# Kernel tuning notes

Hardware: AMD Instinct MI355X
Metric: run time of the kernel (lower is better)

Reference implementation:

```python
import jax, jax.numpy as jnp
import numpy as np

S, N, M, D = 4, 4096, 4096, 128
NEG = -1e30
EPS = 1e-12


def setup_inputs() -> dict:
    key = jax.random.key(0)
    k1, k2, k3 = jax.random.split(key, 3)
    art = jax.random.normal(k1, (S, N, D), dtype=jnp.float32)
    ref = jax.random.normal(k2, (S, M, D), dtype=jnp.float32)
    pos_mask = jax.random.randint(k3, (S, N, M), 0, 2).astype(jnp.bool_)
    log_temperature = jnp.log(jnp.asarray(0.01, dtype=jnp.float32))
    return {"art": art, "ref": ref, "pos_mask": pos_mask, "log_temperature": log_temperature}


def _l2norm(x):
    # F.normalize: x / max(||x||, eps)
    n = jnp.sqrt(jnp.sum(x * x, axis=-1, keepdims=True))
    return x / jnp.maximum(n, EPS)


def reference(art, ref, pos_mask, log_temperature):
    temp = jnp.exp(log_temperature)
    a = _l2norm(art)                                   # [S,N,D]
    r = _l2norm(ref)                                   # [S,M,D]
    logits = jnp.einsum("snd,smd->snm", a, r) / temp   # [S,N,M]

    den = jax.nn.logsumexp(logits, axis=-1)                              # [S,N]
    num = jax.nn.logsumexp(jnp.where(pos_mask, logits, NEG), axis=-1)    # [S,N]

    n_pos = jnp.sum(pos_mask, axis=-1)                 # [S,N]
    n_ref = logits.shape[-1]
    valid = (n_pos > 0) & (n_ref > n_pos)              # skip anchors with 0 pos or all pos

    per_anchor = den - num                             # -(num - den)
    cnt = jnp.sum(valid, axis=-1)                      # [S]
    stem_loss = jnp.sum(jnp.where(valid, per_anchor, 0.0), axis=-1) / jnp.maximum(cnt, 1)
    stem_valid = cnt > 0
    loss = jnp.sum(jnp.where(stem_valid, stem_loss, 0.0)) / jnp.maximum(jnp.sum(stem_valid), 1)
    return loss
```

## Files before the change

kernel.cpp:

```cpp
#include <hip/hip_runtime.h>
#include <hip/hip_bf16.h>
#include <math.h>

#define S_ 4
#define N_ 4096
#define M_ 4096
#define D_ 128
#define NEG_ (-1e30f)
#define CH_ 2
#define MCH_ (M_ / CH_)
#define NST_ (MCH_ / 64)
#define LN2_ 0.69314718055994531f
#define LOG2E_ 1.44269504088896340f

typedef __bf16 bf16x8 __attribute__((ext_vector_type(8)));
typedef float f32x4 __attribute__((ext_vector_type(4)));

__device__ __forceinline__ void gll16(const void* g, void* l) {
    __builtin_amdgcn_global_load_lds(
        (const __attribute__((address_space(1))) unsigned int*)g,
        (__attribute__((address_space(3))) unsigned int*)l, 16, 0, 0);
}

__device__ __forceinline__ unsigned short f2bf(float f) {
    unsigned u = __float_as_uint(f);
    unsigned r = (u + 0x7FFFu + ((u >> 16) & 1u)) >> 16;
    return (unsigned short)r;
}

__global__ void nrm_rows_kernel(const float* __restrict__ art, const float* __restrict__ ref,
                                unsigned short* __restrict__ an, unsigned short* __restrict__ rn) {
    const int w = threadIdx.x >> 6;
    const int lane = threadIdx.x & 63;
    const int row = blockIdx.x * 4 + w;
    const bool is_art = row < S_ * N_;
    const float* src = is_art ? (art + (size_t)row * D_)
                              : (ref + (size_t)(row - S_ * N_) * D_);
    unsigned short* dst = is_art ? (an + (size_t)row * D_)
                                 : (rn + (size_t)(row - S_ * N_) * D_);
    const float2 v = *reinterpret_cast<const float2*>(src + lane * 2);
    float ss = v.x * v.x + v.y * v.y;
#pragma unroll
    for (int off = 1; off < 64; off <<= 1) ss += __shfl_xor(ss, off);
    const float scale = 1.0f / fmaxf(sqrtf(ss), 1e-12f);
    unsigned pack = (unsigned)f2bf(v.x * scale) | ((unsigned)f2bf(v.y * scale) << 16);
    *reinterpret_cast<unsigned*>(dst + lane * 2) = pack;
}

__global__ __launch_bounds__(256, 4) void infonce_main_kernel(
    const unsigned short* __restrict__ an, const unsigned short* __restrict__ rn,
    const unsigned char* __restrict__ maskb, const float* __restrict__ logtemp,
    float4* __restrict__ part4) {

    const int bid = blockIdx.x;
    const int swz = (bid & 7) * 128 + (bid >> 3);
    const int ch = swz >> 9;
    const int s = (swz >> 7) & 3;
    const int nblk = swz & 127;
    const int n_base = nblk * 32;

    const int tid = threadIdx.x;
    const int w = tid >> 6;
    const int lane = tid & 63;
    const int nsub = w & 1;
    const int msub = w >> 1;
    const int n16 = n_base + nsub * 16;
    const int lrow = lane & 15;
    const int lgrp = lane >> 4;
    const float scale2 = __expf(-logtemp[0]) * LOG2E_;

    const unsigned* mu = (const unsigned*)maskb;
    unsigned pr = 0;
#pragma unroll
    for (int i = 0; i < 4; ++i) pr |= (mu[i * 64 + lane] > 1u) ? 1u : 0u;
    const bool byte_mode = (__ballot(pr != 0) != 0ull);
    const size_t mstride = byte_mode ? 1 : 4;

    __shared__ unsigned char smem[2][64 * 256];
    __shared__ unsigned long long mbuf[2][32];
    __shared__ float4 lds4[4][16];

    bf16x8 bfr[4];
    const unsigned short* abase = an + ((size_t)(s * N_ + n16 + lrow)) * D_ + lgrp * 8;
#pragma unroll
    for (int kc = 0; kc < 4; ++kc)
        bfr[kc] = *reinterpret_cast<const bf16x8*>(abase + kc * 32);

    const int srow = w * 4 + (lane >> 4);
    const int schunk = (lane & 15) ^ (srow & 7);
    const int lane_src_off = srow * 256 + schunk * 16;
    const unsigned char* rn_chunk =
        (const unsigned char*)(rn + ((size_t)(s * M_ + ch * MCH_)) * D_);

    size_t rowb[8];
#pragma unroll
    for (int r = 0; r < 8; ++r)
        rowb[r] = ((size_t)(s * N_ + n_base + w * 8 + r) * M_ + (size_t)ch * MCH_) * mstride;

    const int rb0 = (msub * 32 + lrow) * 256;
    int coff[4];
#pragma unroll
    for (int kc = 0; kc < 4; ++kc) coff[kc] = ((kc * 4 + lgrp) ^ (lrow & 7)) * 16;

    float dmax = NEG_, dsum = 0.f, nsum = 0.f;
    int npos = 0;

    {
        const unsigned char* src = rn_chunk + lane_src_off;
        unsigned char* dst = &smem[0][w * 1024];
#pragma unroll
        for (int j = 0; j < 4; ++j) gll16(src + j * 4096, dst + j * 4096);
        unsigned char mv[8];
        const size_t eoff = (size_t)lane * mstride;
#pragma unroll
        for (int r = 0; r < 8; ++r) mv[r] = maskb[rowb[r] + eoff];
        unsigned long long bl[8];
#pragma unroll
        for (int r = 0; r < 8; ++r) bl[r] = __ballot(mv[r] != 0);
        if (lane == 0) {
#pragma unroll
            for (int r = 0; r < 8; ++r) mbuf[0][w * 8 + r] = bl[r];
        }
    }
    __syncthreads();

    for (int st = 0; st < NST_; ++st) {
        const int nb = st & 1;
        const bool pf = (st + 1 < NST_);
        unsigned char mv[8];
        if (pf) {
            const unsigned char* src = rn_chunk + (size_t)(st + 1) * 16384 + lane_src_off;
            unsigned char* dst = &smem[nb ^ 1][w * 1024];
#pragma unroll
            for (int j = 0; j < 4; ++j) gll16(src + j * 4096, dst + j * 4096);
            const size_t eoff = (size_t)((st + 1) * 64 + lane) * mstride;
#pragma unroll
            for (int r = 0; r < 8; ++r) mv[r] = maskb[rowb[r] + eoff];
        }
        const unsigned char* base = &smem[nb][0] + rb0;
        f32x4 acc0 = {0.f, 0.f, 0.f, 0.f}, acc1 = {0.f, 0.f, 0.f, 0.f};
#pragma unroll
        for (int kc = 0; kc < 4; ++kc) {
            acc0 = __builtin_amdgcn_mfma_f32_16x16x32_bf16(
                *reinterpret_cast<const bf16x8*>(base + coff[kc]), bfr[kc], acc0, 0, 0, 0);
            acc1 = __builtin_amdgcn_mfma_f32_16x16x32_bf16(
                *reinterpret_cast<const bf16x8*>(base + 4096 + coff[kc]), bfr[kc], acc1, 0, 0, 0);
        }
        const unsigned long long wmask = mbuf[nb][nsub * 16 + lrow];
        const unsigned nib0 = (unsigned)(wmask >> (msub * 32 + lgrp * 4)) & 0xFu;
        const unsigned nib1 = (unsigned)(wmask >> (msub * 32 + 16 + lgrp * 4)) & 0xFu;
        float l0 = acc0[0] * scale2, l1 = acc0[1] * scale2, l2 = acc0[2] * scale2, l3 = acc0[3] * scale2;
        float l4 = acc1[0] * scale2, l5 = acc1[1] * scale2, l6 = acc1[2] * scale2, l7 = acc1[3] * scale2;
        float tmax = fmaxf(fmaxf(fmaxf(l0, l1), fmaxf(l2, l3)),
                           fmaxf(fmaxf(l4, l5), fmaxf(l6, l7)));
        const float nmx = fmaxf(dmax, tmax);
        const float r = exp2f(dmax - nmx);
        float e0 = exp2f(l0 - nmx), e1 = exp2f(l1 - nmx), e2 = exp2f(l2 - nmx), e3 = exp2f(l3 - nmx);
        float e4 = exp2f(l4 - nmx), e5 = exp2f(l5 - nmx), e6 = exp2f(l6 - nmx), e7 = exp2f(l7 - nmx);
        dsum = dsum * r + (((e0 + e1) + (e2 + e3)) + ((e4 + e5) + (e6 + e7)));
        float p0 = ((nib0 & 1u) ? e0 : 0.f) + (((nib0 >> 1) & 1u) ? e1 : 0.f);
        float p1 = (((nib0 >> 2) & 1u) ? e2 : 0.f) + (((nib0 >> 3) & 1u) ? e3 : 0.f);
        float p2 = ((nib1 & 1u) ? e4 : 0.f) + (((nib1 >> 1) & 1u) ? e5 : 0.f);
        float p3 = (((nib1 >> 2) & 1u) ? e6 : 0.f) + (((nib1 >> 3) & 1u) ? e7 : 0.f);
        nsum = nsum * r + ((p0 + p1) + (p2 + p3));
        npos += __popc(nib0 | (nib1 << 4));
        dmax = nmx;
        if (pf) {
            unsigned long long bl[8];
#pragma unroll
            for (int r2 = 0; r2 < 8; ++r2) bl[r2] = __ballot(mv[r2] != 0);
            if (lane == 0) {
#pragma unroll
                for (int r2 = 0; r2 < 8; ++r2) mbuf[nb ^ 1][w * 8 + r2] = bl[r2];
            }
        }
        __syncthreads();
    }

    float npf = (float)npos;
#pragma unroll
    for (int off = 16; off < 64; off <<= 1) {
        float odm = __shfl_xor(dmax, off), ods = __shfl_xor(dsum, off);
        float ons = __shfl_xor(nsum, off), onp = __shfl_xor(npf, off);
        float nm = fmaxf(dmax, odm);
        float ra = exp2f(dmax - nm), rb = exp2f(odm - nm);
        dsum = dsum * ra + ods * rb;
        nsum = nsum * ra + ons * rb;
        npf += onp;
        dmax = nm;
    }

    if (lane < 16) lds4[w][lane] = make_float4(dmax, dsum, nsum, npf);
    __syncthreads();

    if (w == 0 && lane < 32) {
        const int wsub = lane >> 4;
        const int ni = lane & 15;
        const float4 A = lds4[wsub][ni];
        const float4 B = lds4[wsub + 2][ni];
        const float nm = fmaxf(A.x, B.x);
        const float ra = exp2f(A.x - nm), rb = exp2f(B.x - nm);
        const float ds = A.y * ra + B.y * rb;
        const float ns = A.z * ra + B.z * rb;
        const float np = A.w + B.w;
        const int ag = s * N_ + n_base + wsub * 16 + ni;
        part4[ag * CH_ + ch] = make_float4(nm, ds, ns, np);
    }
}

__global__ void reduce_kernel(const float4* __restrict__ part4, float2* __restrict__ bpart) {
    const int a = blockIdx.x * 256 + threadIdx.x;
    const int w = threadIdx.x >> 6;
    const int lane = threadIdx.x & 63;
    float dm = NEG_, ds = 0.f, ns = 0.f, npf = 0.f;
#pragma unroll
    for (int ch = 0; ch < CH_; ++ch) {
        const float4 p = part4[a * CH_ + ch];
        const float m2 = fmaxf(dm, p.x);
        const float ra = exp2f(dm - m2), rb = exp2f(p.x - m2);
        ds = ds * ra + p.y * rb;
        ns = ns * ra + p.z * rb;
        npf += p.w;
        dm = m2;
    }
    const bool valid = (npf > 0.5f) && (npf < (float)M_ - 0.5f);
    float pa = valid ? LN2_ * (log2f(ds) - log2f(ns)) : 0.f;
    float cv = valid ? 1.f : 0.f;
#pragma unroll
    for (int off = 1; off < 64; off <<= 1) {
        pa += __shfl_xor(pa, off);
        cv += __shfl_xor(cv, off);
    }
    __shared__ float sp[4], sc[4];
    if (lane == 0) { sp[w] = pa; sc[w] = cv; }
    __syncthreads();
    if (threadIdx.x == 0)
        bpart[blockIdx.x] = make_float2(sp[0] + sp[1] + sp[2] + sp[3],
                                        sc[0] + sc[1] + sc[2] + sc[3]);
}

__global__ void finalize_kernel(const float2* __restrict__ bpart, float* __restrict__ out) {
    const int t = threadIdx.x;
    const float2 v = bpart[t];
    float pa = v.x, cv = v.y;
#pragma unroll
    for (int off = 1; off < 16; off <<= 1) {
        pa += __shfl_xor(pa, off);
        cv += __shfl_xor(cv, off);
    }
    const float p0 = __shfl(pa, 0),  c0 = __shfl(cv, 0);
    const float p1 = __shfl(pa, 16), c1 = __shfl(cv, 16);
    const float p2 = __shfl(pa, 32), c2 = __shfl(cv, 32);
    const float p3 = __shfl(pa, 48), c3 = __shfl(cv, 48);
    if (t == 0) {
        float total = 0.f;
        int scnt = 0;
        const float ps[4] = {p0, p1, p2, p3};
        const float cs[4] = {c0, c1, c2, c3};
        for (int s = 0; s < S_; ++s) {
            const float stem = ps[s] / fmaxf(cs[s], 1.f);
            if (cs[s] > 0.f) { total += stem; scnt++; }
        }
        out[0] = total / (float)(scnt > 0 ? scnt : 1);
    }
}

extern "C" void kernel_launch(void* const* d_in, const int* in_sizes, int n_in,
                              void* d_out, int out_size, void* d_ws, size_t ws_size,
                              hipStream_t stream) {
    const float* art = (const float*)d_in[0];
    const float* ref = (const float*)d_in[1];
    const unsigned char* mask = (const unsigned char*)d_in[2];
    const float* lt = (const float*)d_in[3];
    float* out = (float*)d_out;

    char* ws = (char*)d_ws;
    unsigned short* an = (unsigned short*)ws;
    unsigned short* rn = (unsigned short*)(ws + (size_t)4194304);
    float4* part4 = (float4*)(ws + (size_t)8388608);
    float2* bpart = (float2*)(ws + (size_t)9437184);

    nrm_rows_kernel<<<(S_ * (N_ + M_)) / 4, 256, 0, stream>>>(art, ref, an, rn);
    infonce_main_kernel<<<S_ * (N_ / 32) * CH_, 256, 0, stream>>>(an, rn, mask, lt, part4);
    reduce_kernel<<<(S_ * N_) / 256, 256, 0, stream>>>(part4, bpart);
    finalize_kernel<<<1, 64, 0, stream>>>(bpart, out);
}
```

Before: 409.9 us.

## Prefetch mask bytes two stages ahead with manual vmcnt waits; widen normalize loads

The main loop is unrolled by two with ping-pong mask registers, so mask bytes are loaded two stages ahead and the LDS tile one stage ahead. __syncthreads is replaced by explicit s_waitcnt vmcnt(8) plus s_barrier, so the outstanding mask loads stay in flight across the barrier. The normalize kernel now handles two rows per wave using float4 loads and 32-lane reductions. This hides mask-load latency, which dominates this memory-bound loop, at the cost of more registers and hand-tuned wait counts that could break correctness if they are miscounted.

```diff
diff --git a/kernel.cpp b/kernel.cpp
--- a/kernel.cpp
+++ b/kernel.cpp
@@ -32,19 +32,23 @@
                                 unsigned short* __restrict__ an, unsigned short* __restrict__ rn) {
     const int w = threadIdx.x >> 6;
     const int lane = threadIdx.x & 63;
-    const int row = blockIdx.x * 4 + w;
+    const int half = lane >> 5;
+    const int li = lane & 31;
+    const int row = blockIdx.x * 8 + w * 2 + half;
     const bool is_art = row < S_ * N_;
     const float* src = is_art ? (art + (size_t)row * D_)
                               : (ref + (size_t)(row - S_ * N_) * D_);
     unsigned short* dst = is_art ? (an + (size_t)row * D_)
                                  : (rn + (size_t)(row - S_ * N_) * D_);
-    const float2 v = *reinterpret_cast<const float2*>(src + lane * 2);
-    float ss = v.x * v.x + v.y * v.y;
-#pragma unroll
-    for (int off = 1; off < 64; off <<= 1) ss += __shfl_xor(ss, off);
+    const float4 v = *reinterpret_cast<const float4*>(src + li * 4);
+    float ss = v.x * v.x + v.y * v.y + v.z * v.z + v.w * v.w;
+#pragma unroll
+    for (int off = 1; off < 32; off <<= 1) ss += __shfl_xor(ss, off);
     const float scale = 1.0f / fmaxf(sqrtf(ss), 1e-12f);
-    unsigned pack = (unsigned)f2bf(v.x * scale) | ((unsigned)f2bf(v.y * scale) << 16);
-    *reinterpret_cast<unsigned*>(dst + lane * 2) = pack;
+    uint2 pack;
+    pack.x = (unsigned)f2bf(v.x * scale) | ((unsigned)f2bf(v.y * scale) << 16);
+    pack.y = (unsigned)f2bf(v.z * scale) | ((unsigned)f2bf(v.w * scale) << 16);
+    *reinterpret_cast<uint2*>(dst + li * 4) = pack;
 }
 
 __global__ __launch_bounds__(256, 4) void infonce_main_kernel(
@@ -104,78 +108,101 @@
 
     float dmax = NEG_, dsum = 0.f, nsum = 0.f;
     int npos = 0;
+    unsigned mvA[8], mvB[8];
 
     {
         const unsigned char* src = rn_chunk + lane_src_off;
         unsigned char* dst = &smem[0][w * 1024];
 #pragma unroll
         for (int j = 0; j < 4; ++j) gll16(src + j * 4096, dst + j * 4096);
-        unsigned char mv[8];
-        const size_t eoff = (size_t)lane * mstride;
-#pragma unroll
-        for (int r = 0; r < 8; ++r) mv[r] = maskb[rowb[r] + eoff];
+        __builtin_amdgcn_sched_barrier(0);
+        unsigned char m0[8];
+        const size_t e0 = (size_t)lane * mstride;
+#pragma unroll
+        for (int r = 0; r < 8; ++r) m0[r] = maskb[rowb[r] + e0];
         unsigned long long bl[8];
 #pragma unroll
-        for (int r = 0; r < 8; ++r) bl[r] = __ballot(mv[r] != 0);
+        for (int r = 0; r < 8; ++r) bl[r] = __ballot(m0[r] != 0);
         if (lane == 0) {
 #pragma unroll
             for (int r = 0; r < 8; ++r) mbuf[0][w * 8 + r] = bl[r];
         }
-    }
-    __syncthreads();
-
-    for (int st = 0; st < NST_; ++st) {
-        const int nb = st & 1;
-        const bool pf = (st + 1 < NST_);
-        unsigned char mv[8];
-        if (pf) {
-            const unsigned char* src = rn_chunk + (size_t)(st + 1) * 16384 + lane_src_off;
-            unsigned char* dst = &smem[nb ^ 1][w * 1024];
-#pragma unroll
-            for (int j = 0; j < 4; ++j) gll16(src + j * 4096, dst + j * 4096);
-            const size_t eoff = (size_t)((st + 1) * 64 + lane) * mstride;
-#pragma unroll
-            for (int r = 0; r < 8; ++r) mv[r] = maskb[rowb[r] + eoff];
-        }
-        const unsigned char* base = &smem[nb][0] + rb0;
-        f32x4 acc0 = {0.f, 0.f, 0.f, 0.f}, acc1 = {0.f, 0.f, 0.f, 0.f};
-#pragma unroll
-        for (int kc = 0; kc < 4; ++kc) {
-            acc0 = __builtin_amdgcn_mfma_f32_16x16x32_bf16(
-                *reinterpret_cast<const bf16x8*>(base + coff[kc]), bfr[kc], acc0, 0, 0, 0);
-            acc1 = __builtin_amdgcn_mfma_f32_16x16x32_bf16(
-                *reinterpret_cast<const bf16x8*>(base + 4096 + coff[kc]), bfr[kc], acc1, 0, 0, 0);
-        }
-        const unsigned long long wmask = mbuf[nb][nsub * 16 + lrow];
-        const unsigned nib0 = (unsigned)(wmask >> (msub * 32 + lgrp * 4)) & 0xFu;
-        const unsigned nib1 = (unsigned)(wmask >> (msub * 32 + 16 + lgrp * 4)) & 0xFu;
-        float l0 = acc0[0] * scale2, l1 = acc0[1] * scale2, l2 = acc0[2] * scale2, l3 = acc0[3] * scale2;
-        float l4 = acc1[0] * scale2, l5 = acc1[1] * scale2, l6 = acc1[2] * scale2, l7 = acc1[3] * scale2;
-        float tmax = fmaxf(fmaxf(fmaxf(l0, l1), fmaxf(l2, l3)),
-                           fmaxf(fmaxf(l4, l5), fmaxf(l6, l7)));
-        const float nmx = fmaxf(dmax, tmax);
-        const float r = exp2f(dmax - nmx);
-        float e0 = exp2f(l0 - nmx), e1 = exp2f(l1 - nmx), e2 = exp2f(l2 - nmx), e3 = exp2f(l3 - nmx);
-        float e4 = exp2f(l4 - nmx), e5 = exp2f(l5 - nmx), e6 = exp2f(l6 - nmx), e7 = exp2f(l7 - nmx);
-        dsum = dsum * r + (((e0 + e1) + (e2 + e3)) + ((e4 + e5) + (e6 + e7)));
-        float p0 = ((nib0 & 1u) ? e0 : 0.f) + (((nib0 >> 1) & 1u) ? e1 : 0.f);
-        float p1 = (((nib0 >> 2) & 1u) ? e2 : 0.f) + (((nib0 >> 3) & 1u) ? e3 : 0.f);
-        float p2 = ((nib1 & 1u) ? e4 : 0.f) + (((nib1 >> 1) & 1u) ? e5 : 0.f);
-        float p3 = (((nib1 >> 2) & 1u) ? e6 : 0.f) + (((nib1 >> 3) & 1u) ? e7 : 0.f);
-        nsum = nsum * r + ((p0 + p1) + (p2 + p3));
-        npos += __popc(nib0 | (nib1 << 4));
-        dmax = nmx;
-        if (pf) {
-            unsigned long long bl[8];
-#pragma unroll
-            for (int r2 = 0; r2 < 8; ++r2) bl[r2] = __ballot(mv[r2] != 0);
-            if (lane == 0) {
-#pragma unroll
-                for (int r2 = 0; r2 < 8; ++r2) mbuf[nb ^ 1][w * 8 + r2] = bl[r2];
-            }
-        }
-        __syncthreads();
-    }
+        const size_t e1 = (size_t)(64 + lane) * mstride;
+#pragma unroll
+        for (int r = 0; r < 8; ++r) mvA[r] = maskb[rowb[r] + e1];
+        asm volatile("s_waitcnt vmcnt(8)" ::: "memory");
+        __builtin_amdgcn_s_barrier();
+    }
+
+#define STAGE(ST, MVU, MVL, DOG, DOM, WAITSTR)                                          \
+    {                                                                                   \
+        const int nb_ = (ST) & 1;                                                       \
+        if (DOG) {                                                                      \
+            const unsigned char* src_ = rn_chunk + (size_t)((ST) + 1) * 16384 + lane_src_off; \
+            unsigned char* dst_ = &smem[nb_ ^ 1][w * 1024];                             \
+            _Pragma("unroll")                                                           \
+            for (int j = 0; j < 4; ++j) gll16(src_ + j * 4096, dst_ + j * 4096);        \
+        }                                                                               \
+        __builtin_amdgcn_sched_barrier(0);                                              \
+        if (DOM) {                                                                      \
+            const size_t eo_ = (size_t)(((ST) + 2) * 64 + lane) * mstride;              \
+            _Pragma("unroll")                                                           \
+            for (int r = 0; r < 8; ++r) MVL[r] = maskb[rowb[r] + eo_];                  \
+        }                                                                               \
+        const unsigned char* base_ = &smem[nb_][0] + rb0;                               \
+        f32x4 acc0 = {0.f, 0.f, 0.f, 0.f}, acc1 = {0.f, 0.f, 0.f, 0.f};                 \
+        _Pragma("unroll")                                                               \
+        for (int kc = 0; kc < 4; ++kc) {                                                \
+            acc0 = __builtin_amdgcn_mfma_f32_16x16x32_bf16(                             \
+                *reinterpret_cast<const bf16x8*>(base_ + coff[kc]), bfr[kc], acc0, 0, 0, 0); \
+            acc1 = __builtin_amdgcn_mfma_f32_16x16x32_bf16(                             \
+                *reinterpret_cast<const bf16x8*>(base_ + 4096 + coff[kc]), bfr[kc], acc1, 0, 0, 0); \
+        }                                                                               \
+        const unsigned long long wmask = mbuf[nb_][nsub * 16 + lrow];                   \
+        const unsigned nib0 = (unsigned)(wmask >> (msub * 32 + lgrp * 4)) & 0xFu;       \
+        const unsigned nib1 = (unsigned)(wmask >> (msub * 32 + 16 + lgrp * 4)) & 0xFu;  \
+        float l0 = acc0[0] * scale2, l1 = acc0[1] * scale2;                             \
+        float l2 = acc0[2] * scale2, l3 = acc0[3] * scale2;                             \
+        float l4 = acc1[0] * scale2, l5 = acc1[1] * scale2;                             \
+        float l6 = acc1[2] * scale2, l7 = acc1[3] * scale2;                             \
+        float tmax = fmaxf(fmaxf(fmaxf(l0, l1), fmaxf(l2, l3)),                         \
+                           fmaxf(fmaxf(l4, l5), fmaxf(l6, l7)));                        \
+        const float nmx = fmaxf(dmax, tmax);                                            \
+        const float r_ = exp2f(dmax - nmx);                                             \
+        float e0 = exp2f(l0 - nmx), e1 = exp2f(l1 - nmx);                               \
+        float e2 = exp2f(l2 - nmx), e3 = exp2f(l3 - nmx);                               \
+        float e4 = exp2f(l4 - nmx), e5 = exp2f(l5 - nmx);                               \
+        float e6 = exp2f(l6 - nmx), e7 = exp2f(l7 - nmx);                               \
+        dsum = dsum * r_ + (((e0 + e1) + (e2 + e3)) + ((e4 + e5) + (e6 + e7)));         \
+        float p0 = ((nib0 & 1u) ? e0 : 0.f) + (((nib0 >> 1) & 1u) ? e1 : 0.f);          \
+        float p1 = (((nib0 >> 2) & 1u) ? e2 : 0.f) + (((nib0 >> 3) & 1u) ? e3 : 0.f);   \
+        float p2 = ((nib1 & 1u) ? e4 : 0.f) + (((nib1 >> 1) & 1u) ? e5 : 0.f);          \
+        float p3 = (((nib1 >> 2) & 1u) ? e6 : 0.f) + (((nib1 >> 3) & 1u) ? e7 : 0.f);   \
+        nsum = nsum * r_ + ((p0 + p1) + (p2 + p3));                                     \
+        npos += __popc(nib0 | (nib1 << 4));                                             \
+        dmax = nmx;                                                                     \
+        if (DOG) {                                                                      \
+            unsigned long long bl_[8];                                                  \
+            _Pragma("unroll")                                                           \
+            for (int r2 = 0; r2 < 8; ++r2) bl_[r2] = __ballot(MVU[r2] != 0);            \
+            if (lane == 0) {                                                            \
+                _Pragma("unroll")                                                       \
+                for (int r2 = 0; r2 < 8; ++r2) mbuf[nb_ ^ 1][w * 8 + r2] = bl_[r2];     \
+            }                                                                           \
+        }                                                                               \
+        asm volatile(WAITSTR ::: "memory");                                             \
+        __builtin_amdgcn_s_barrier();                                                   \
+    }
+
+    for (int st = 0; st < NST_ - 4; st += 2) {
+        STAGE(st,     mvA, mvB, true, true, "s_waitcnt vmcnt(8)");
+        STAGE(st + 1, mvB, mvA, true, true, "s_waitcnt vmcnt(8)");
+    }
+    STAGE(NST_ - 4, mvA, mvB, true,  true,  "s_waitcnt vmcnt(8)");
+    STAGE(NST_ - 3, mvB, mvA, true,  true,  "s_waitcnt vmcnt(8)");
+    STAGE(NST_ - 2, mvA, mvB, true,  false, "s_waitcnt vmcnt(0)");
+    STAGE(NST_ - 1, mvB, mvA, false, false, "s_waitcnt vmcnt(0)");
+#undef STAGE
 
     float npf = (float)npos;
 #pragma unroll
@@ -280,7 +307,7 @@
     float4* part4 = (float4*)(ws + (size_t)8388608);
     float2* bpart = (float2*)(ws + (size_t)9437184);
 
-    nrm_rows_kernel<<<(S_ * (N_ + M_)) / 4, 256, 0, stream>>>(art, ref, an, rn);
+    nrm_rows_kernel<<<(S_ * (N_ + M_)) / 8, 256, 0, stream>>>(art, ref, an, rn);
     infonce_main_kernel<<<S_ * (N_ / 32) * CH_, 256, 0, stream>>>(an, rn, mask, lt, part4);
     reduce_kernel<<<(S_ * N_) / 256, 256, 0, stream>>>(part4, bpart);
     finalize_kernel<<<1, 64, 0, stream>>>(bpart, out);
```

After: 412.2 us. No clear change (+0.6%).

## Vectorize mask loads with 4-step grouped prefetch into LDS nibble buffer

Applied to the files above, without the earlier changes.

The mask is now read as wide vectors (int or int4 per lane covering four columns) over groups of four M-tiles, and packed into per-row nibbles in a double-buffered LDS array. This replaces the per-element byte loads and ballots issued on every tile. The mask element size becomes a template parameter, so each mode gets its own specialised code path. The normalise kernel now handles two rows per wave with float4 loads. The cost is more registers held for the prefetched mask and a larger LDS footprint, which may reduce occupancy.

```diff
diff --git a/kernel.cpp b/kernel.cpp
--- a/kernel.cpp
+++ b/kernel.cpp
@@ -10,6 +10,7 @@
 #define CH_ 2
 #define MCH_ (M_ / CH_)
 #define NST_ (MCH_ / 64)
+#define NGRP_ (NST_ / 4)
 #define LN2_ 0.69314718055994531f
 #define LOG2E_ 1.44269504088896340f
 
@@ -32,32 +33,52 @@
                                 unsigned short* __restrict__ an, unsigned short* __restrict__ rn) {
     const int w = threadIdx.x >> 6;
     const int lane = threadIdx.x & 63;
-    const int row = blockIdx.x * 4 + w;
+    const int half = lane >> 5;
+    const int li = lane & 31;
+    const int row = blockIdx.x * 8 + w * 2 + half;
     const bool is_art = row < S_ * N_;
     const float* src = is_art ? (art + (size_t)row * D_)
                               : (ref + (size_t)(row - S_ * N_) * D_);
     unsigned short* dst = is_art ? (an + (size_t)row * D_)
                                  : (rn + (size_t)(row - S_ * N_) * D_);
-    const float2 v = *reinterpret_cast<const float2*>(src + lane * 2);
-    float ss = v.x * v.x + v.y * v.y;
-#pragma unroll
-    for (int off = 1; off < 64; off <<= 1) ss += __shfl_xor(ss, off);
+    const float4 v = *reinterpret_cast<const float4*>(src + li * 4);
+    float ss = v.x * v.x + v.y * v.y + v.z * v.z + v.w * v.w;
+#pragma unroll
+    for (int off = 1; off < 32; off <<= 1) ss += __shfl_xor(ss, off);
     const float scale = 1.0f / fmaxf(sqrtf(ss), 1e-12f);
-    unsigned pack = (unsigned)f2bf(v.x * scale) | ((unsigned)f2bf(v.y * scale) << 16);
-    *reinterpret_cast<unsigned*>(dst + lane * 2) = pack;
-}
-
-__global__ __launch_bounds__(256, 4) void infonce_main_kernel(
+    uint2 pack;
+    pack.x = (unsigned)f2bf(v.x * scale) | ((unsigned)f2bf(v.y * scale) << 16);
+    pack.y = (unsigned)f2bf(v.z * scale) | ((unsigned)f2bf(v.w * scale) << 16);
+    *reinterpret_cast<uint2*>(dst + li * 4) = pack;
+}
+
+template <int ESZ>
+__device__ __forceinline__ void mload(int4* mq, const unsigned char* __restrict__ maskb,
+                                      const size_t* rowb, int g, int lane) {
+#pragma unroll
+    for (int r = 0; r < 8; ++r) {
+        const unsigned char* p = maskb + rowb[r] + (size_t)((g * 256 + 4 * lane) * ESZ);
+        if (ESZ == 4) mq[r] = *reinterpret_cast<const int4*>(p);
+        else          mq[r].x = *reinterpret_cast<const int*>(p);
+    }
+}
+
+template <int ESZ>
+__device__ __forceinline__ unsigned nib_of(const int4 q) {
+    if (ESZ == 4)
+        return (unsigned)((q.x != 0) | ((q.y != 0) << 1) | ((q.z != 0) << 2) | ((q.w != 0) << 3));
+    const unsigned b = (unsigned)q.x;
+    return (((b & 0xFFu) != 0) ? 1u : 0u) | (((b >> 8) & 0xFFu) ? 2u : 0u)
+         | (((b >> 16) & 0xFFu) ? 4u : 0u) | ((b >> 24) ? 8u : 0u);
+}
+
+template <int ESZ>
+__device__ __forceinline__ void run_main(
     const unsigned short* __restrict__ an, const unsigned short* __restrict__ rn,
-    const unsigned char* __restrict__ maskb, const float* __restrict__ logtemp,
-    float4* __restrict__ part4) {
-
-    const int bid = blockIdx.x;
-    const int swz = (bid & 7) * 128 + (bid >> 3);
-    const int ch = swz >> 9;
-    const int s = (swz >> 7) & 3;
-    const int nblk = swz & 127;
-    const int n_base = nblk * 32;
+    const unsigned char* __restrict__ maskb, float scale2, float4* __restrict__ part4,
+    int s, int ch, int n_base,
+    unsigned char (&smem)[2][64 * 256], unsigned char (&mnib)[2][32][68],
+    float4 (&lds4)[4][16]) {
 
     const int tid = threadIdx.x;
     const int w = tid >> 6;
@@ -67,18 +88,6 @@
     const int n16 = n_base + nsub * 16;
     const int lrow = lane & 15;
     const int lgrp = lane >> 4;
-    const float scale2 = __expf(-logtemp[0]) * LOG2E_;
-
-    const unsigned* mu = (const unsigned*)maskb;
-    unsigned pr = 0;
-#pragma unroll
-    for (int i = 0; i < 4; ++i) pr |= (mu[i * 64 + lane] > 1u) ? 1u : 0u;
-    const bool byte_mode = (__ballot(pr != 0) != 0ull);
-    const size_t mstride = byte_mode ? 1 : 4;
-
-    __shared__ unsigned char smem[2][64 * 256];
-    __shared__ unsigned long long mbuf[2][32];
-    __shared__ float4 lds4[4][16];
 
     bf16x8 bfr[4];
     const unsigned short* abase = an + ((size_t)(s * N_ + n16 + lrow)) * D_ + lgrp * 8;
@@ -95,7 +104,7 @@
     size_t rowb[8];
 #pragma unroll
     for (int r = 0; r < 8; ++r)
-        rowb[r] = ((size_t)(s * N_ + n_base + w * 8 + r) * M_ + (size_t)ch * MCH_) * mstride;
+        rowb[r] = ((size_t)(s * N_ + n_base + w * 8 + r) * M_ + (size_t)ch * MCH_) * ESZ;
 
     const int rb0 = (msub * 32 + lrow) * 256;
     int coff[4];
@@ -104,77 +113,73 @@
 
     float dmax = NEG_, dsum = 0.f, nsum = 0.f;
     int npos = 0;
+    int4 mq[8];
 
     {
         const unsigned char* src = rn_chunk + lane_src_off;
         unsigned char* dst = &smem[0][w * 1024];
 #pragma unroll
         for (int j = 0; j < 4; ++j) gll16(src + j * 4096, dst + j * 4096);
-        unsigned char mv[8];
-        const size_t eoff = (size_t)lane * mstride;
-#pragma unroll
-        for (int r = 0; r < 8; ++r) mv[r] = maskb[rowb[r] + eoff];
-        unsigned long long bl[8];
-#pragma unroll
-        for (int r = 0; r < 8; ++r) bl[r] = __ballot(mv[r] != 0);
-        if (lane == 0) {
-#pragma unroll
-            for (int r = 0; r < 8; ++r) mbuf[0][w * 8 + r] = bl[r];
+        mload<ESZ>(mq, maskb, rowb, 0, lane);
+#pragma unroll
+        for (int r = 0; r < 8; ++r)
+            mnib[0][w * 8 + r][lane] = (unsigned char)nib_of<ESZ>(mq[r]);
+        mload<ESZ>(mq, maskb, rowb, 1, lane);
+        __syncthreads();
+    }
+
+    for (int g = 0; g < NGRP_; ++g) {
+#pragma unroll
+        for (int j = 0; j < 4; ++j) {
+            const int st = g * 4 + j;
+            const int nb = j & 1;
+            if (j < 3 || g < NGRP_ - 1) {
+                const unsigned char* src_ = rn_chunk + (size_t)(st + 1) * 16384 + lane_src_off;
+                unsigned char* dst_ = &smem[nb ^ 1][w * 1024];
+#pragma unroll
+                for (int jj = 0; jj < 4; ++jj) gll16(src_ + jj * 4096, dst_ + jj * 4096);
+            }
+            if (j == 3 && g < NGRP_ - 1) {
+#pragma unroll
+                for (int r = 0; r < 8; ++r)
+                    mnib[(g + 1) & 1][w * 8 + r][lane] = (unsigned char)nib_of<ESZ>(mq[r]);
+                if (g < NGRP_ - 2) mload<ESZ>(mq, maskb, rowb, g + 2, lane);
+            }
+            const unsigned char* base_ = &smem[nb][0] + rb0;
+            f32x4 acc0 = {0.f, 0.f, 0.f, 0.f}, acc1 = {0.f, 0.f, 0.f, 0.f};
+#pragma unroll
+            for (int kc = 0; kc < 4; ++kc) {
+                acc0 = __builtin_amdgcn_mfma_f32_16x16x32_bf16(
+                    *reinterpret_cast<const bf16x8*>(base_ + coff[kc]), bfr[kc], acc0, 0, 0, 0);
+                acc1 = __builtin_amdgcn_mfma_f32_16x16x32_bf16(
+                    *reinterpret_cast<const bf16x8*>(base_ + 4096 + coff[kc]), bfr[kc], acc1, 0, 0, 0);
+            }
+            const int row = nsub * 16 + lrow;
+            const int nidx = j * 16 + msub * 8 + lgrp;
+            const unsigned nib0 = mnib[g & 1][row][nidx];
+            const unsigned nib1 = mnib[g & 1][row][nidx + 4];
+            float l0 = acc0[0] * scale2, l1 = acc0[1] * scale2;
+            float l2 = acc0[2] * scale2, l3 = acc0[3] * scale2;
+            float l4 = acc1[0] * scale2, l5 = acc1[1] * scale2;
+            float l6 = acc1[2] * scale2, l7 = acc1[3] * scale2;
+            float tmax = fmaxf(fmaxf(fmaxf(l0, l1), fmaxf(l2, l3)),
+                               fmaxf(fmaxf(l4, l5), fmaxf(l6, l7)));
+            const float nmx = fmaxf(dmax, tmax);
+            const float r_ = exp2f(dmax - nmx);
+            float e0 = exp2f(l0 - nmx), e1 = exp2f(l1 - nmx);
+            float e2 = exp2f(l2 - nmx), e3 = exp2f(l3 - nmx);
+            float e4 = exp2f(l4 - nmx), e5 = exp2f(l5 - nmx);
+            float e6 = exp2f(l6 - nmx), e7 = exp2f(l7 - nmx);
+            dsum = dsum * r_ + (((e0 + e1) + (e2 + e3)) + ((e4 + e5) + (e6 + e7)));
+            float p0 = ((nib0 & 1u) ? e0 : 0.f) + (((nib0 >> 1) & 1u) ? e1 : 0.f);
+            float p1 = (((nib0 >> 2) & 1u) ? e2 : 0.f) + (((nib0 >> 3) & 1u) ? e3 : 0.f);
+            float p2 = ((nib1 & 1u) ? e4 : 0.f) + (((nib1 >> 1) & 1u) ? e5 : 0.f);
+            float p3 = (((nib1 >> 2) & 1u) ? e6 : 0.f) + (((nib1 >> 3) & 1u) ? e7 : 0.f);
+            nsum = nsum * r_ + ((p0 + p1) + (p2 + p3));
+            npos += __popc(nib0 | (nib1 << 4));
+            dmax = nmx;
+            __syncthreads();
         }
-    }
-    __syncthreads();
-
-    for (int st = 0; st < NST_; ++st) {
-        const int nb = st & 1;
-        const bool pf = (st + 1 < NST_);
-        unsigned char mv[8];
-        if (pf) {
-            const unsigned char* src = rn_chunk + (size_t)(st + 1) * 16384 + lane_src_off;
-            unsigned char* dst = &smem[nb ^ 1][w * 1024];
-#pragma unroll
-            for (int j = 0; j < 4; ++j) gll16(src + j * 4096, dst + j * 4096);
-            const size_t eoff = (size_t)((st + 1) * 64 + lane) * mstride;
-#pragma unroll
-            for (int r = 0; r < 8; ++r) mv[r] = maskb[rowb[r] + eoff];
-        }
-        const unsigned char* base = &smem[nb][0] + rb0;
-        f32x4 acc0 = {0.f, 0.f, 0.f, 0.f}, acc1 = {0.f, 0.f, 0.f, 0.f};
-#pragma unroll
-        for (int kc = 0; kc < 4; ++kc) {
-            acc0 = __builtin_amdgcn_mfma_f32_16x16x32_bf16(
-                *reinterpret_cast<const bf16x8*>(base + coff[kc]), bfr[kc], acc0, 0, 0, 0);
-            acc1 = __builtin_amdgcn_mfma_f32_16x16x32_bf16(
-                *reinterpret_cast<const bf16x8*>(base + 4096 + coff[kc]), bfr[kc], acc1, 0, 0, 0);
-        }
-        const unsigned long long wmask = mbuf[nb][nsub * 16 + lrow];
-        const unsigned nib0 = (unsigned)(wmask >> (msub * 32 + lgrp * 4)) & 0xFu;
-        const unsigned nib1 = (unsigned)(wmask >> (msub * 32 + 16 + lgrp * 4)) & 0xFu;
-        float l0 = acc0[0] * scale2, l1 = acc0[1] * scale2, l2 = acc0[2] * scale2, l3 = acc0[3] * scale2;
-        float l4 = acc1[0] * scale2, l5 = acc1[1] * scale2, l6 = acc1[2] * scale2, l7 = acc1[3] * scale2;
-        float tmax = fmaxf(fmaxf(fmaxf(l0, l1), fmaxf(l2, l3)),
-                           fmaxf(fmaxf(l4, l5), fmaxf(l6, l7)));
-        const float nmx = fmaxf(dmax, tmax);
-        const float r = exp2f(dmax - nmx);
-        float e0 = exp2f(l0 - nmx), e1 = exp2f(l1 - nmx), e2 = exp2f(l2 - nmx), e3 = exp2f(l3 - nmx);
-        float e4 = exp2f(l4 - nmx), e5 = exp2f(l5 - nmx), e6 = exp2f(l6 - nmx), e7 = exp2f(l7 - nmx);
-        dsum = dsum * r + (((e0 + e1) + (e2 + e3)) + ((e4 + e5) + (e6 + e7)));
-        float p0 = ((nib0 & 1u) ? e0 : 0.f) + (((nib0 >> 1) & 1u) ? e1 : 0.f);
-        float p1 = (((nib0 >> 2) & 1u) ? e2 : 0.f) + (((nib0 >> 3) & 1u) ? e3 : 0.f);
-        float p2 = ((nib1 & 1u) ? e4 : 0.f) + (((nib1 >> 1) & 1u) ? e5 : 0.f);
-        float p3 = (((nib1 >> 2) & 1u) ? e6 : 0.f) + (((nib1 >> 3) & 1u) ? e7 : 0.f);
-        nsum = nsum * r + ((p0 + p1) + (p2 + p3));
-        npos += __popc(nib0 | (nib1 << 4));
-        dmax = nmx;
-        if (pf) {
-            unsigned long long bl[8];
-#pragma unroll
-            for (int r2 = 0; r2 < 8; ++r2) bl[r2] = __ballot(mv[r2] != 0);
-            if (lane == 0) {
-#pragma unroll
-                for (int r2 = 0; r2 < 8; ++r2) mbuf[nb ^ 1][w * 8 + r2] = bl[r2];
-            }
-        }
-        __syncthreads();
     }
 
     float npf = (float)npos;
@@ -206,6 +211,34 @@
         const int ag = s * N_ + n_base + wsub * 16 + ni;
         part4[ag * CH_ + ch] = make_float4(nm, ds, ns, np);
     }
+}
+
+__global__ __launch_bounds__(256, 4) void infonce_main_kernel(
+    const unsigned short* __restrict__ an, const unsigned short* __restrict__ rn,
+    const unsigned char* __restrict__ maskb, const float* __restrict__ logtemp,
+    float4* __restrict__ part4) {
+
+    const int bid = blockIdx.x;
+    const int swz = (bid & 7) * 128 + (bid >> 3);
+    const int ch = swz >> 9;
+    const int s = (swz >> 7) & 3;
+    const int n_base = (swz & 127) * 32;
+    const float scale2 = __expf(-logtemp[0]) * LOG2E_;
+
+    const unsigned* mu = (const unsigned*)maskb;
+    unsigned pr = 0;
+#pragma unroll
+    for (int i = 0; i < 4; ++i) pr |= (mu[i * 64 + (threadIdx.x & 63)] > 1u) ? 1u : 0u;
+    const bool byte_mode = (__ballot(pr != 0) != 0ull);
+
+    __shared__ unsigned char smem[2][64 * 256];
+    __shared__ unsigned char mnib[2][32][68];
+    __shared__ float4 lds4[4][16];
+
+    if (byte_mode)
+        run_main<1>(an, rn, maskb, scale2, part4, s, ch, n_base, smem, mnib, lds4);
+    else
+        run_main<4>(an, rn, maskb, scale2, part4, s, ch, n_base, smem, mnib, lds4);
 }
 
 __global__ void reduce_kernel(const float4* __restrict__ part4, float2* __restrict__ bpart) {
@@ -280,7 +313,7 @@
     float4* part4 = (float4*)(ws + (size_t)8388608);
     float2* bpart = (float2*)(ws + (size_t)9437184);
 
-    nrm_rows_kernel<<<(S_ * (N_ + M_)) / 4, 256, 0, stream>>>(art, ref, an, rn);
+    nrm_rows_kernel<<<(S_ * (N_ + M_)) / 8, 256, 0, stream>>>(art, ref, an, rn);
     infonce_main_kernel<<<S_ * (N_ / 32) * CH_, 256, 0, stream>>>(an, rn, mask, lt, part4);
     reduce_kernel<<<(S_ * N_) / 256, 256, 0, stream>>>(part4, bpart);
     finalize_kernel<<<1, 64, 0, stream>>>(bpart, out);
```

Measured after the change: 400.3 us. 2.3% less time.
